# Kernel tuning notes

Hardware: AMD Instinct MI355X
Metric: run time of the kernel (lower is better)

## Reference

```python
import jax, jax.numpy as jnp
import numpy as np

S, B, D, H, MLP_H, W = 2048, 4, 1024, 16, 4096, 16
EPS = 1e-6

def _ln(x):
    m = jnp.mean(x, axis=-1, keepdims=True)
    v = jnp.var(x, axis=-1, keepdims=True)
    return (x - m) / jnp.sqrt(v + EPS)

def setup_inputs() -> dict:
    key = jax.random.key(0)
    ks = jax.random.split(key, 12)
    sc = lambda k, shape, fan: jax.random.normal(k, shape, jnp.float32) / np.sqrt(fan)
    return {
        'x': jax.random.normal(ks[0], (S, B, D), jnp.float32),
        'c': jax.random.normal(ks[1], (B, D), jnp.float32),
        'ada_w': sc(ks[2], (6 * D, D), D),
        'ada_b': jax.random.normal(ks[3], (6 * D,), jnp.float32) * 0.02,
        'in_proj_w': sc(ks[4], (3 * D, D), D),
        'in_proj_b': jax.random.normal(ks[5], (3 * D,), jnp.float32) * 0.02,
        'out_proj_w': sc(ks[6], (D, D), D),
        'out_proj_b': jax.random.normal(ks[7], (D,), jnp.float32) * 0.02,
        'mlp_w1': sc(ks[8], (MLP_H, D), D),
        'mlp_b1': jax.random.normal(ks[9], (MLP_H,), jnp.float32) * 0.02,
        'mlp_w2': sc(ks[10], (D, MLP_H), MLP_H),
        'mlp_b2': jax.random.normal(ks[11], (D,), jnp.float32) * 0.02,
        'num_heads': H,
        'window_size': W,
    }

def _attn(x, in_proj_w, in_proj_b, out_proj_w, out_proj_b, num_heads, window_size):
    s, b, d = x.shape
    dh = d // num_heads
    qkv = x @ in_proj_w.T + in_proj_b            # [S,B,3D]
    q, k, v = jnp.split(qkv, 3, axis=-1)
    def heads(t):  # [S,B,D] -> [B,H,S,dh]
        return t.reshape(s, b, num_heads, dh).transpose(1, 2, 0, 3)
    q, k, v = heads(q), heads(k), heads(v)
    scores = jnp.einsum('bhsd,bhtd->bhst', q, k) / np.sqrt(dh)
    idx = jnp.arange(s)
    band = jnp.abs(idx[:, None] - idx[None, :]) <= window_size  # [S,S]
    scores = jnp.where(band[None, None], scores, -jnp.inf)
    attn = jax.nn.softmax(scores, axis=-1)
    o = jnp.einsum('bhst,bhtd->bhsd', attn, v)   # [B,H,S,dh]
    o = o.transpose(2, 0, 1, 3).reshape(s, b, d)
    return o @ out_proj_w.T + out_proj_b

def reference(x, c, ada_w, ada_b, in_proj_w, in_proj_b, out_proj_w, out_proj_b, mlp_w1, mlp_b1, mlp_w2, mlp_b2, num_heads, window_size):
    mod = jax.nn.relu(c) @ ada_w.T + ada_b       # [B,6D]
    sh_msa, sc_msa, g_msa, sh_mlp, sc_mlp, g_mlp = jnp.split(mod, 6, axis=1)
    xm = _ln(x) * (1.0 + sc_msa[None]) + sh_msa[None]
    x = x + g_msa[None] * _attn(xm, in_proj_w, in_proj_b, out_proj_w, out_proj_b, num_heads, window_size)
    xm = _ln(x) * (1.0 + sc_mlp[None]) + sh_mlp[None]
    h = jax.nn.relu(xm @ mlp_w1.T + mlp_b1)
    mlp_out = h @ mlp_w2.T + mlp_b2
    return x + g_mlp[None] * mlp_out
```

## Files before the change

### kernel.cpp

```cpp
#include <hip/hip_runtime.h>

#define S_LEN 2048
#define BATCH 4
#define DMODEL 1024
#define NHEAD 16
#define MROWS (S_LEN * BATCH)
#define MOD6 (6 * DMODEL)

typedef float f32x4 __attribute__((ext_vector_type(4)));
typedef short bf16x8 __attribute__((ext_vector_type(8)));
typedef unsigned short ushort_t;

__device__ __forceinline__ unsigned short f2bf(float f) {
  unsigned u = __float_as_uint(f);
  u += 0x7FFF + ((u >> 16) & 1);
  return (unsigned short)(u >> 16);
}
__device__ __forceinline__ float bf2f(unsigned short h) {
  return __uint_as_float(((unsigned)h) << 16);
}
__device__ __forceinline__ float wave_sum(float v) {
#pragma unroll
  for (int off = 32; off > 0; off >>= 1) v += __shfl_xor(v, off, 64);
  return v;
}
__device__ __forceinline__ void mfma16(f32x4& c, bf16x8 a, bf16x8 b) {
  asm volatile("v_mfma_f32_16x16x32_bf16 %0, %1, %2, %0" : "+v"(c) : "v"(a), "v"(b));
}
__device__ __forceinline__ void mfma_fence() {
  __builtin_amdgcn_sched_barrier(0);
  asm volatile("s_nop 7\n\ts_nop 7\n\ts_nop 7");
  __builtin_amdgcn_sched_barrier(0);
}
__device__ __forceinline__ void async16(const void* g, void* l) {
  __builtin_amdgcn_global_load_lds((const __attribute__((address_space(1))) void*)g,
                                   (__attribute__((address_space(3))) void*)l, 16, 0, 0);
}

__launch_bounds__(256)
__global__ void castk(const float4* __restrict__ in, ushort4* __restrict__ out, int n4) {
  int i = blockIdx.x * 256 + threadIdx.x;
  if (i < n4) {
    float4 v = in[i];
    ushort4 o;
    o.x = f2bf(v.x); o.y = f2bf(v.y); o.z = f2bf(v.z); o.w = f2bf(v.w);
    out[i] = o;
  }
}

__launch_bounds__(256)
__global__ void ada_k(const float* __restrict__ c, const float* __restrict__ aw,
                      const float* __restrict__ ab, float* __restrict__ mod) {
  int j = blockIdx.x;
  int b = threadIdx.x >> 6;
  int l = threadIdx.x & 63;
  const float* wrow = aw + (size_t)j * DMODEL;
  const float* crow = c + b * DMODEL;
  float s = 0.f;
#pragma unroll 4
  for (int i = l; i < DMODEL; i += 64) {
    float cv = crow[i];
    cv = cv > 0.f ? cv : 0.f;
    s += cv * wrow[i];
  }
  s = wave_sum(s);
  if (l == 0) mod[b * MOD6 + j] = s + ab[j];
}

__launch_bounds__(256)
__global__ void ln_mod(const float* __restrict__ x, const float* __restrict__ mod,
                       int sh_off, int sc_off, ushort_t* __restrict__ out) {
  __shared__ float red[8];
  int row = blockIdx.x;
  int b = row & 3;
  int tid = threadIdx.x;
  const float4* xr = (const float4*)(x + (size_t)row * DMODEL);
  float4 v = xr[tid];
  float s = v.x + v.y + v.z + v.w;
  float s2 = v.x * v.x + v.y * v.y + v.z * v.z + v.w * v.w;
  s = wave_sum(s);
  s2 = wave_sum(s2);
  int w = tid >> 6, l = tid & 63;
  if (l == 0) { red[w] = s; red[4 + w] = s2; }
  __syncthreads();
  s = red[0] + red[1] + red[2] + red[3];
  s2 = red[4] + red[5] + red[6] + red[7];
  float mean = s * (1.0f / DMODEL);
  float var = s2 * (1.0f / DMODEL) - mean * mean;
  float inv = rsqrtf(var + 1e-6f);
  const float* shp = mod + b * MOD6 + sh_off;
  const float* scp = mod + b * MOD6 + sc_off;
  float vv[4] = {v.x, v.y, v.z, v.w};
  ushort4 ov;
  ushort_t* op = (ushort_t*)&ov;
#pragma unroll
  for (int j = 0; j < 4; j++) {
    int idx = tid * 4 + j;
    float y = (vv[j] - mean) * inv * (1.0f + scp[idx]) + shp[idx];
    op[j] = f2bf(y);
  }
  ((ushort4*)(out + (size_t)row * DMODEL))[tid] = ov;
}

__launch_bounds__(256)
__global__ void attn_mfma(const ushort_t* __restrict__ qkv, ushort_t* __restrict__ out) {
  const int l = threadIdx.x & 63;
  const int widx = blockIdx.x * 4 + (threadIdx.x >> 6);
  const int qblk = widx & 63;
  const int bh = widx >> 6;
  const int h = bh & 15;
  const int b = bh >> 4;
  const int q0 = qblk * 32;
  int k0 = q0 - 16;
  if (k0 < 0) k0 = 0;
  if (k0 > S_LEN - 64) k0 = S_LEN - 64;
  const int lr = l & 15;
  const int g = l >> 4;

  const char* base = (const char*)qkv;

  bf16x8 qf[2][2], kf[4][2];
#pragma unroll
  for (int nt = 0; nt < 2; nt++) {
    size_t rowb = (size_t)((q0 + 16 * nt + lr) * 4 + b) * 6144 + h * 128 + 16 * g;
#pragma unroll
    for (int ks = 0; ks < 2; ks++)
      qf[nt][ks] = *(const bf16x8*)(base + rowb + 64 * ks);
  }
#pragma unroll
  for (int mt = 0; mt < 4; mt++) {
    size_t rowb = (size_t)((k0 + 16 * mt + lr) * 4 + b) * 6144 + 2048 + h * 128 + 16 * g;
#pragma unroll
    for (int ks = 0; ks < 2; ks++)
      kf[mt][ks] = *(const bf16x8*)(base + rowb + 64 * ks);
  }

  f32x4 acc[4][2] = {};
#pragma unroll
  for (int mt = 0; mt < 4; mt++)
#pragma unroll
    for (int nt = 0; nt < 2; nt++)
#pragma unroll
      for (int ks = 0; ks < 2; ks++)
        mfma16(acc[mt][nt], kf[mt][ks], qf[nt][ks]);
  mfma_fence();

  float p0[16], p1[16];
  const int sq0 = q0 + lr, sq1 = q0 + 16 + lr;
  float m0 = -1e30f, m1 = -1e30f;
#pragma unroll
  for (int mt = 0; mt < 4; mt++)
#pragma unroll
    for (int i = 0; i < 4; i++) {
      int sk = k0 + 16 * mt + 4 * g + i;
      int d0 = sq0 - sk, d1 = sq1 - sk;
      float s0 = (d0 <= 16 && d0 >= -16) ? acc[mt][0][i] * 0.125f : -1e30f;
      float s1 = (d1 <= 16 && d1 >= -16) ? acc[mt][1][i] * 0.125f : -1e30f;
      p0[mt * 4 + i] = s0;
      p1[mt * 4 + i] = s1;
      m0 = fmaxf(m0, s0);
      m1 = fmaxf(m1, s1);
    }
  m0 = fmaxf(m0, __shfl_xor(m0, 16, 64));
  m0 = fmaxf(m0, __shfl_xor(m0, 32, 64));
  m1 = fmaxf(m1, __shfl_xor(m1, 16, 64));
  m1 = fmaxf(m1, __shfl_xor(m1, 32, 64));
  float l0 = 0.f, l1 = 0.f;
#pragma unroll
  for (int j = 0; j < 16; j++) {
    float e0 = __expf(p0[j] - m0);
    float e1 = __expf(p1[j] - m1);
    p0[j] = e0; p1[j] = e1;
    l0 += e0; l1 += e1;
  }
  l0 += __shfl_xor(l0, 16, 64); l0 += __shfl_xor(l0, 32, 64);
  l1 += __shfl_xor(l1, 16, 64); l1 += __shfl_xor(l1, 32, 64);
  const float inv0 = 1.0f / l0, inv1 = 1.0f / l1;

  const size_t vb = (size_t)b * 6144 + 4096 + h * 128;
  for (int c = 0; c < 8; c++) {
    float o0[8] = {}, o1[8] = {};
#pragma unroll
    for (int mt = 0; mt < 4; mt++)
#pragma unroll
      for (int i = 0; i < 4; i++) {
        int t = k0 + 16 * mt + 4 * g + i;
        bf16x8 v = *(const bf16x8*)(base + (size_t)t * 24576 + vb + 16 * c);
        float pa = p0[mt * 4 + i], pb = p1[mt * 4 + i];
#pragma unroll
        for (int d = 0; d < 8; d++) {
          float vf = bf2f((unsigned short)v[d]);
          o0[d] += pa * vf;
          o1[d] += pb * vf;
        }
      }
#pragma unroll
    for (int d = 0; d < 8; d++) {
      o0[d] += __shfl_xor(o0[d], 16, 64); o0[d] += __shfl_xor(o0[d], 32, 64);
      o1[d] += __shfl_xor(o1[d], 16, 64); o1[d] += __shfl_xor(o1[d], 32, 64);
    }
    if (g < 2) {
      int sq = q0 + 16 * g + lr;
      bf16x8 ov;
#pragma unroll
      for (int d = 0; d < 8; d++) {
        float val = (g ? o1[d] : o0[d]) * (g ? inv1 : inv0);
        ov[d] = (short)f2bf(val);
      }
      *(bf16x8*)((char*)out + (size_t)(sq * 4 + b) * 2048 + h * 128 + c * 16) = ov;
    }
  }
}

template <int EPI>
__launch_bounds__(256)
__global__ void gemm_bt(const ushort_t* __restrict__ A, const ushort_t* __restrict__ W,
                        const float* __restrict__ bias, const float* __restrict__ res,
                        const float* __restrict__ gmod, void* __restrict__ outp,
                        int M, int N, int K) {
  __shared__ alignas(16) ushort_t As[128 * 64];
  __shared__ alignas(16) ushort_t Bs[128 * 64];
  const int tid = threadIdx.x;
  const int w = tid >> 6;
  const int l = tid & 63;
  const int row0 = blockIdx.y * 128;
  const int col0 = blockIdx.x * 128;
  const int wr = (w >> 1) * 64;
  const int wc = (w & 1) * 64;

  f32x4 acc[4][4] = {};

  const int srow = tid >> 3;
  const int scc = (((tid & 7) ^ (srow & 7)) << 3);
  const ushort_t* ga = A + (size_t)(row0 + srow) * K + scc;
  const ushort_t* gb = W + (size_t)(col0 + srow) * K + scc;
  char* lA = (char*)As + w * 1024;
  char* lB = (char*)Bs + w * 1024;

  const int lrow = l & 15;
  const int g = l >> 4;
  const int cx0 = ((g ^ (lrow & 7)) << 4);
  const int cx1 = (((4 + g) ^ (lrow & 7)) << 4);
  const int arow = (wr + lrow) * 128;
  const int brow = (wc + lrow) * 128;

  const int nk = K >> 6;
  for (int it = 0; it < nk; ++it) {
#pragma unroll
    for (int r = 0; r < 4; r++) async16(ga + (size_t)(32 * r) * K, lA + r * 4096);
#pragma unroll
    for (int r = 0; r < 4; r++) async16(gb + (size_t)(32 * r) * K, lB + r * 4096);
    ga += 64;
    gb += 64;
    __syncthreads();
#pragma unroll
    for (int kk = 0; kk < 2; kk++) {
      const int cx = kk ? cx1 : cx0;
      bf16x8 afr[4], bfr[4];
#pragma unroll
      for (int m = 0; m < 4; m++) afr[m] = *(const bf16x8*)((char*)As + arow + m * 2048 + cx);
#pragma unroll
      for (int n = 0; n < 4; n++) bfr[n] = *(const bf16x8*)((char*)Bs + brow + n * 2048 + cx);
#pragma unroll
      for (int m = 0; m < 4; m++)
#pragma unroll
        for (int n = 0; n < 4; n++) mfma16(acc[m][n], afr[m], bfr[n]);
    }
    __syncthreads();
  }
  mfma_fence();

  const int crow = row0 + wr + g * 4;
  const int ccol = col0 + wc + lrow;
#pragma unroll
  for (int m = 0; m < 4; m++) {
#pragma unroll
    for (int i = 0; i < 4; i++) {
      int grow = crow + m * 16 + i;
#pragma unroll
      for (int n = 0; n < 4; n++) {
        int gcol = ccol + n * 16;
        float v = acc[m][n][i] + bias[gcol];
        if constexpr (EPI == 0) {
          ((ushort_t*)outp)[(size_t)grow * N + gcol] = f2bf(v);
        } else if constexpr (EPI == 1) {
          ((ushort_t*)outp)[(size_t)grow * N + gcol] = f2bf(v > 0.f ? v : 0.f);
        } else {
          int bb = grow & 3;
          ((float*)outp)[(size_t)grow * N + gcol] =
              res[(size_t)grow * N + gcol] + gmod[bb * MOD6 + gcol] * v;
        }
      }
    }
  }
}

extern "C" void kernel_launch(void* const* d_in, const int* in_sizes, int n_in,
                              void* d_out, int out_size, void* d_ws, size_t ws_size,
                              hipStream_t stream) {
  const float* x     = (const float*)d_in[0];
  const float* c     = (const float*)d_in[1];
  const float* ada_w = (const float*)d_in[2];
  const float* ada_b = (const float*)d_in[3];
  const float* in_w  = (const float*)d_in[4];
  const float* in_b  = (const float*)d_in[5];
  const float* out_w = (const float*)d_in[6];
  const float* out_b = (const float*)d_in[7];
  const float* w1    = (const float*)d_in[8];
  const float* b1    = (const float*)d_in[9];
  const float* w2    = (const float*)d_in[10];
  const float* b2    = (const float*)d_in[11];

  char* ws = (char*)d_ws;
  float* mod    = (float*)ws;
  ushort_t* wq  = (ushort_t*)(ws + 98304);
  ushort_t* wo  = (ushort_t*)(ws + 6389760);
  ushort_t* wm1 = (ushort_t*)(ws + 8486912);
  ushort_t* wm2 = (ushort_t*)(ws + 16875520);
  ushort_t* xm  = (ushort_t*)(ws + 25264128);
  ushort_t* qkv = (ushort_t*)(ws + 42041344);
  ushort_t* att = (ushort_t*)(ws + 92372992);
  ushort_t* h   = (ushort_t*)(ws + 42041344);
  float* x1 = (float*)d_out;

  castk<<<(3072 * 1024 / 4 + 255) / 256, 256, 0, stream>>>((const float4*)in_w, (ushort4*)wq, 3072 * 1024 / 4);
  castk<<<(1024 * 1024 / 4 + 255) / 256, 256, 0, stream>>>((const float4*)out_w, (ushort4*)wo, 1024 * 1024 / 4);
  castk<<<(4096 * 1024 / 4 + 255) / 256, 256, 0, stream>>>((const float4*)w1, (ushort4*)wm1, 4096 * 1024 / 4);
  castk<<<(1024 * 4096 / 4 + 255) / 256, 256, 0, stream>>>((const float4*)w2, (ushort4*)wm2, 1024 * 4096 / 4);

  ada_k<<<MOD6, 256, 0, stream>>>(c, ada_w, ada_b, mod);

  ln_mod<<<MROWS, 256, 0, stream>>>(x, mod, 0, 1024, xm);
  gemm_bt<0><<<dim3(3072 / 128, MROWS / 128), 256, 0, stream>>>(xm, wq, in_b, nullptr, nullptr, qkv, MROWS, 3072, 1024);
  attn_mfma<<<(BATCH * NHEAD * (S_LEN / 32)) / 4, 256, 0, stream>>>(qkv, att);
  gemm_bt<2><<<dim3(1024 / 128, MROWS / 128), 256, 0, stream>>>(att, wo, out_b, x, mod + 2 * DMODEL, x1, MROWS, 1024, 1024);
  ln_mod<<<MROWS, 256, 0, stream>>>(x1, mod, 3 * DMODEL, 4 * DMODEL, xm);
  gemm_bt<1><<<dim3(4096 / 128, MROWS / 128), 256, 0, stream>>>(xm, wm1, b1, nullptr, nullptr, h, MROWS, 4096, 1024);
  gemm_bt<2><<<dim3(1024 / 128, MROWS / 128), 256, 0, stream>>>(h, wm2, b2, x1, mod + 5 * DMODEL, (float*)d_out, MROWS, 1024, 4096);
}
```

Measured before the change: 328.6 us.

## Template GEMM on K, remap workgroups across XCDs, raise occupancy, set MFMA priority

Makes K a compile-time template parameter so the GEMM K-loop can be fully specialised. It remaps linear workgroup IDs in strides of eight so adjacent tiles land on the same XCD and share its L2. It adds a minimum-occupancy hint of 4 blocks per CU to launch_bounds. It raises wave priority around the attention QK MFMA block. The occupancy hint may force register limits and cause spills, and the remap changes which tiles run concurrently.

```diff
diff --git a/kernel.cpp b/kernel.cpp
--- a/kernel.cpp
+++ b/kernel.cpp
@@ -136,6 +136,7 @@
   }
 
   f32x4 acc[4][2] = {};
+  __builtin_amdgcn_s_setprio(1);
 #pragma unroll
   for (int mt = 0; mt < 4; mt++)
 #pragma unroll
@@ -143,6 +144,7 @@
 #pragma unroll
       for (int ks = 0; ks < 2; ks++)
         mfma16(acc[mt][nt], kf[mt][ks], qf[nt][ks]);
+  __builtin_amdgcn_s_setprio(0);
   mfma_fence();
 
   float p0[16], p1[16];
@@ -212,19 +214,31 @@
   }
 }
 
-template <int EPI>
-__launch_bounds__(256)
+template <int EPI, int K>
+__launch_bounds__(256, 4)
 __global__ void gemm_bt(const ushort_t* __restrict__ A, const ushort_t* __restrict__ W,
                         const float* __restrict__ bias, const float* __restrict__ res,
                         const float* __restrict__ gmod, void* __restrict__ outp,
-                        int M, int N, int K) {
+                        int M, int N) {
   __shared__ alignas(16) ushort_t As[128 * 64];
   __shared__ alignas(16) ushort_t Bs[128 * 64];
   const int tid = threadIdx.x;
   const int w = tid >> 6;
   const int l = tid & 63;
-  const int row0 = blockIdx.y * 128;
-  const int col0 = blockIdx.x * 128;
+
+  int bx = blockIdx.x, by = blockIdx.y;
+  {
+    const int nbx = gridDim.x;
+    const int nwg = nbx * gridDim.y;
+    if ((nwg & 7) == 0) {
+      int lin = by * nbx + bx;
+      int nlin = (lin & 7) * (nwg >> 3) + (lin >> 3);
+      bx = nlin % nbx;
+      by = nlin / nbx;
+    }
+  }
+  const int row0 = by * 128;
+  const int col0 = bx * 128;
   const int wr = (w >> 1) * 64;
   const int wc = (w & 1) * 64;
 
@@ -331,10 +345,10 @@
   ada_k<<<MOD6, 256, 0, stream>>>(c, ada_w, ada_b, mod);
 
   ln_mod<<<MROWS, 256, 0, stream>>>(x, mod, 0, 1024, xm);
-  gemm_bt<0><<<dim3(3072 / 128, MROWS / 128), 256, 0, stream>>>(xm, wq, in_b, nullptr, nullptr, qkv, MROWS, 3072, 1024);
+  gemm_bt<0, 1024><<<dim3(3072 / 128, MROWS / 128), 256, 0, stream>>>(xm, wq, in_b, nullptr, nullptr, qkv, MROWS, 3072);
   attn_mfma<<<(BATCH * NHEAD * (S_LEN / 32)) / 4, 256, 0, stream>>>(qkv, att);
-  gemm_bt<2><<<dim3(1024 / 128, MROWS / 128), 256, 0, stream>>>(att, wo, out_b, x, mod + 2 * DMODEL, x1, MROWS, 1024, 1024);
+  gemm_bt<2, 1024><<<dim3(1024 / 128, MROWS / 128), 256, 0, stream>>>(att, wo, out_b, x, mod + 2 * DMODEL, x1, MROWS, 1024);
   ln_mod<<<MROWS, 256, 0, stream>>>(x1, mod, 3 * DMODEL, 4 * DMODEL, xm);
-  gemm_bt<1><<<dim3(4096 / 128, MROWS / 128), 256, 0, stream>>>(xm, wm1, b1, nullptr, nullptr, h, MROWS, 4096, 1024);
-  gemm_bt<2><<<dim3(1024 / 128, MROWS / 128), 256, 0, stream>>>(h, wm2, b2, x1, mod + 5 * DMODEL, (float*)d_out, MROWS, 1024, 4096);
-}
+  gemm_bt<1, 1024><<<dim3(4096 / 128, MROWS / 128), 256, 0, stream>>>(xm, wm1, b1, nullptr, nullptr, h, MROWS, 4096);
+  gemm_bt<2, 4096><<<dim3(1024 / 128, MROWS / 128), 256, 0, stream>>>(h, wm2, b2, x1, mod + 5 * DMODEL, (float*)d_out, MROWS, 1024);
+}
```

New measurement: 323.2 us. Within noise of the previous version (-1.7%).
